# Performance work log

Measured on AMD Instinct MI355X. Metric: run time of the kernel, lower is better.

## Reference

```python
import jax, jax.numpy as jnp
import numpy as np

# Paired binary-tree layout over 20 inputs: widths 20->10->5->3->2->1.
# Odd trailing element is carried through unchanged. Node counts per layer
# sum to 19 nodes per tree; 19 trees total.
LAYER_WIDTHS = [20, 10, 5, 3, 2]  # widths at the input of each pairing layer
NODE_COUNTS = [10, 5, 2, 1, 1]    # pairs formed at each layer (sum = 19)
EPS = 1e-6


def setup_inputs() -> dict:
    key = jax.random.key(0)
    k1, k2, k3, k4 = jax.random.split(key, 4)
    B = 1_000_000
    p1 = jax.random.randint(k1, (B,), 0, 10)
    p2 = jax.random.randint(k2, (B,), 0, 10)
    c20 = jax.random.uniform(k3, (B, 20), dtype=jnp.float32)  # fuzzy truth values in [0,1]
    # raw andness params: one per node (19) per tree (19)
    w_raw = jax.random.normal(k4, (19, 19), dtype=jnp.float32)
    return {"p1": p1, "p2": p2, "c20": c20, "w_raw": w_raw}


def _multi_tree_forward(c20, w_raw):
    B = c20.shape[0]
    T = 19  # number of trees
    # andness in (0,1): convex mix between AND (min) and OR (max)
    w = jax.nn.sigmoid(w_raw)  # [T, 19]
    # all 19 trees see the same 20D input -> vectorize trees as a dim
    x = jnp.broadcast_to(c20[:, None, :], (B, T, 20))  # [B, T, 20]
    off = 0
    for width, n in zip(LAYER_WIDTHS, NODE_COUNTS):
        a = x[:, :, 0:2 * n:2]   # left children  [B, T, n]
        b = x[:, :, 1:2 * n:2]   # right children [B, T, n]
        wn = w[:, off:off + n][None, :, :]  # [1, T, n]
        y = wn * jnp.minimum(a, b) + (1.0 - wn) * jnp.maximum(a, b)
        if width % 2 == 1:  # carry the unpaired trailing element through
            y = jnp.concatenate([y, x[:, :, -1:]], axis=-1)
        x = y
        off += n
    out = x[:, :, 0]  # [B, 19] root of each tree
    return jnp.clip(out, EPS, 1.0 - EPS)


def reference(p1, p2, c20, w_raw):
    # p1/p2 are part of the original signature but unused by the forward math
    return _multi_tree_forward(c20, w_raw)
```

## Files before the change

### kernel.cpp

```cpp
#include <hip/hip_runtime.h>

#define EPS_F 1e-6f
#define BLK   256

typedef float v4f __attribute__((ext_vector_type(4)));

__global__ void sigmoid_w_kernel(const float* __restrict__ w_raw,
                                 float* __restrict__ w) {
    int i = threadIdx.x;
    if (i < 361) {
        w[i] = 1.0f / (1.0f + expf(-w_raw[i]));
    }
}

__device__ __forceinline__ float mixf(float a, float b, float wv) {
    float mn = fminf(a, b);
    float mx = fmaxf(a, b);
    return fmaf(wv, mn - mx, mx);
}

__device__ __forceinline__ float clampf(float r) {
    return __builtin_amdgcn_fmed3f(r, EPS_F, 1.0f - EPS_F);
}

__global__ __launch_bounds__(BLK, 4) void tree_forward_kernel(
    const float* __restrict__ c20,
    const float* __restrict__ w,
    float* __restrict__ out,
    int B)
{
    __shared__ float si[BLK * 20];
    __shared__ float so[BLK * 19];

    const int tid = threadIdx.x;
    const int S0  = blockIdx.x * BLK;

    {
        const v4f* g4 = reinterpret_cast<const v4f*>(c20) + (size_t)S0 * 5;
        v4f* s4 = reinterpret_cast<v4f*>(si);
        const int lim4  = B * 5;
        const int base4 = S0 * 5;
        #pragma unroll
        for (int j = 0; j < 5; ++j) {
            int idx = tid + j * BLK;
            v4f v;
            if (base4 + idx < lim4) {
                v = g4[idx];
            } else {
                v.x = 0.f; v.y = 0.f; v.z = 0.f; v.w = 0.f;
            }
            s4[idx] = v;
        }
    }
    __syncthreads();

    float mx[10], d[10];
    {
        const v4f* r4 = reinterpret_cast<const v4f*>(si + tid * 20);
        #pragma unroll
        for (int q = 0; q < 5; ++q) {
            v4f v = r4[q];
            {
                float mn = fminf(v.x, v.y);
                mx[2*q] = fmaxf(v.x, v.y);
                d[2*q]  = mn - mx[2*q];
            }
            {
                float mn = fminf(v.z, v.w);
                mx[2*q+1] = fmaxf(v.z, v.w);
                d[2*q+1]  = mn - mx[2*q+1];
            }
        }
    }

    float* __restrict__ o = &so[tid * 19];

    #pragma unroll
    for (int tp = 0; tp < 9; ++tp) {
        const int t0 = 2 * tp, t1 = 2 * tp + 1;
        const float* wr0 = w + t0 * 19;
        const float* wr1 = w + t1 * 19;

        float y0[10], y1[10];
        #pragma unroll
        for (int k = 0; k < 10; ++k) {
            y0[k] = fmaf(wr0[k], d[k], mx[k]);
            y1[k] = fmaf(wr1[k], d[k], mx[k]);
        }

        float z0[5], z1[5];
        #pragma unroll
        for (int k = 0; k < 5; ++k) {
            z0[k] = mixf(y0[2*k], y0[2*k+1], wr0[10 + k]);
            z1[k] = mixf(y1[2*k], y1[2*k+1], wr1[10 + k]);
        }

        float u00 = mixf(z0[0], z0[1], wr0[15]);
        float u01 = mixf(z0[2], z0[3], wr0[16]);
        float u10 = mixf(z1[0], z1[1], wr1[15]);
        float u11 = mixf(z1[2], z1[3], wr1[16]);

        float v0 = mixf(u00, u01, wr0[17]);
        float v1 = mixf(u10, u11, wr1[17]);

        float r0 = mixf(v0, z0[4], wr0[18]);
        float r1 = mixf(v1, z1[4], wr1[18]);

        o[t0] = clampf(r0);
        o[t1] = clampf(r1);
    }

    {
        const float* wr = w + 18 * 19;
        float y[10];
        #pragma unroll
        for (int k = 0; k < 10; ++k)
            y[k] = fmaf(wr[k], d[k], mx[k]);
        float z[5];
        #pragma unroll
        for (int k = 0; k < 5; ++k)
            z[k] = mixf(y[2*k], y[2*k+1], wr[10 + k]);
        float u0 = mixf(z[0], z[1], wr[15]);
        float u1 = mixf(z[2], z[3], wr[16]);
        float v0 = mixf(u0, u1, wr[17]);
        float r  = mixf(v0, z[4], wr[18]);
        o[18] = clampf(r);
    }

    __syncthreads();

    const int nDw    = B * 19;
    const int baseDw = S0 * 19;
    const v4f* ls = reinterpret_cast<const v4f*>(so);

    #pragma unroll
    for (int i = tid; i < (BLK * 19) / 4; i += BLK) {
        int g = baseDw + i * 4;
        if (g + 3 < nDw) {
            __builtin_nontemporal_store(ls[i], reinterpret_cast<v4f*>(out + g));
        } else if (g < nDw) {
            v4f v4 = ls[i];
            out[g] = v4.x;
            if (g + 1 < nDw) out[g + 1] = v4.y;
            if (g + 2 < nDw) out[g + 2] = v4.z;
        }
    }
}

extern "C" void kernel_launch(void* const* d_in, const int* in_sizes, int n_in,
                              void* d_out, int out_size, void* d_ws, size_t ws_size,
                              hipStream_t stream) {
    const float* c20   = (const float*)d_in[2];
    const float* w_raw = (const float*)d_in[3];
    float* out = (float*)d_out;
    float* w   = (float*)d_ws;

    int B = in_sizes[0];

    sigmoid_w_kernel<<<1, 384, 0, stream>>>(w_raw, w);

    int grid = (B + BLK - 1) / BLK;
    tree_forward_kernel<<<grid, BLK, 0, stream>>>(c20, w, out, B);
}
```

Measured before the change: 159.7 us.

## Load inputs directly per thread, process two samples per thread, wave-local output staging

Drops the shared-memory staging of the input rows. Each thread now loads its own 20-float rows straight from global memory with vector loads, and processes two samples (512 per block), with both rows' loads issued up front. Output is still staged in shared memory, but each wave copies out only its own 64 rows under wave barriers instead of a block-wide __syncthreads. The aim is to remove block syncs and an LDS round-trip and to raise memory-level parallelism. The cost is strided, uncoalesced 80-byte-per-thread global loads, more registers, and a reliance on the LDS write-then-read ordering holding within a wave.

```diff
diff --git a/kernel.cpp b/kernel.cpp
--- a/kernel.cpp
+++ b/kernel.cpp
@@ -2,6 +2,7 @@
 
 #define EPS_F 1e-6f
 #define BLK   256
+#define TPB   512
 
 typedef float v4f __attribute__((ext_vector_type(4)));
 
@@ -23,58 +24,26 @@
     return __builtin_amdgcn_fmed3f(r, EPS_F, 1.0f - EPS_F);
 }
 
-__global__ __launch_bounds__(BLK, 4) void tree_forward_kernel(
-    const float* __restrict__ c20,
-    const float* __restrict__ w,
-    float* __restrict__ out,
-    int B)
-{
-    __shared__ float si[BLK * 20];
-    __shared__ float so[BLK * 19];
-
-    const int tid = threadIdx.x;
-    const int S0  = blockIdx.x * BLK;
-
-    {
-        const v4f* g4 = reinterpret_cast<const v4f*>(c20) + (size_t)S0 * 5;
-        v4f* s4 = reinterpret_cast<v4f*>(si);
-        const int lim4  = B * 5;
-        const int base4 = S0 * 5;
-        #pragma unroll
-        for (int j = 0; j < 5; ++j) {
-            int idx = tid + j * BLK;
-            v4f v;
-            if (base4 + idx < lim4) {
-                v = g4[idx];
-            } else {
-                v.x = 0.f; v.y = 0.f; v.z = 0.f; v.w = 0.f;
-            }
-            s4[idx] = v;
+__device__ __forceinline__ void layer0(const v4f in[5], float d[10], float mx[10]) {
+    #pragma unroll
+    for (int q = 0; q < 5; ++q) {
+        v4f v = in[q];
+        {
+            float mn = fminf(v.x, v.y);
+            mx[2*q] = fmaxf(v.x, v.y);
+            d[2*q]  = mn - mx[2*q];
+        }
+        {
+            float mn = fminf(v.z, v.w);
+            mx[2*q+1] = fmaxf(v.z, v.w);
+            d[2*q+1]  = mn - mx[2*q+1];
         }
     }
-    __syncthreads();
+}
 
-    float mx[10], d[10];
-    {
-        const v4f* r4 = reinterpret_cast<const v4f*>(si + tid * 20);
-        #pragma unroll
-        for (int q = 0; q < 5; ++q) {
-            v4f v = r4[q];
-            {
-                float mn = fminf(v.x, v.y);
-                mx[2*q] = fmaxf(v.x, v.y);
-                d[2*q]  = mn - mx[2*q];
-            }
-            {
-                float mn = fminf(v.z, v.w);
-                mx[2*q+1] = fmaxf(v.z, v.w);
-                d[2*q+1]  = mn - mx[2*q+1];
-            }
-        }
-    }
-
-    float* __restrict__ o = &so[tid * 19];
-
+__device__ __forceinline__ void trees19(const float* __restrict__ w,
+                                        const float d[10], const float mx[10],
+                                        float* __restrict__ dst) {
     #pragma unroll
     for (int tp = 0; tp < 9; ++tp) {
         const int t0 = 2 * tp, t1 = 2 * tp + 1;
@@ -87,29 +56,23 @@
             y0[k] = fmaf(wr0[k], d[k], mx[k]);
             y1[k] = fmaf(wr1[k], d[k], mx[k]);
         }
-
         float z0[5], z1[5];
         #pragma unroll
         for (int k = 0; k < 5; ++k) {
             z0[k] = mixf(y0[2*k], y0[2*k+1], wr0[10 + k]);
             z1[k] = mixf(y1[2*k], y1[2*k+1], wr1[10 + k]);
         }
-
         float u00 = mixf(z0[0], z0[1], wr0[15]);
         float u01 = mixf(z0[2], z0[3], wr0[16]);
         float u10 = mixf(z1[0], z1[1], wr1[15]);
         float u11 = mixf(z1[2], z1[3], wr1[16]);
-
         float v0 = mixf(u00, u01, wr0[17]);
         float v1 = mixf(u10, u11, wr1[17]);
-
         float r0 = mixf(v0, z0[4], wr0[18]);
         float r1 = mixf(v1, z1[4], wr1[18]);
-
-        o[t0] = clampf(r0);
-        o[t1] = clampf(r1);
+        dst[t0] = clampf(r0);
+        dst[t1] = clampf(r1);
     }
-
     {
         const float* wr = w + 18 * 19;
         float y[10];
@@ -124,27 +87,82 @@
         float u1 = mixf(z[2], z[3], wr[16]);
         float v0 = mixf(u0, u1, wr[17]);
         float r  = mixf(v0, z[4], wr[18]);
-        o[18] = clampf(r);
+        dst[18] = clampf(r);
+    }
+}
+
+__device__ __forceinline__ void waveCopyOut(const float* __restrict__ soW,
+                                            float* __restrict__ out,
+                                            int baseDw, int nDw, int ln) {
+    const v4f* ls = reinterpret_cast<const v4f*>(soW);
+    #pragma unroll
+    for (int j = 0; j < 5; ++j) {
+        int idx = ln + j * 64;
+        if (idx < 304) {
+            int g = baseDw + idx * 4;
+            if (g + 3 < nDw) {
+                __builtin_nontemporal_store(ls[idx], reinterpret_cast<v4f*>(out + g));
+            } else if (g < nDw) {
+                v4f t = ls[idx];
+                out[g] = t.x;
+                if (g + 1 < nDw) out[g + 1] = t.y;
+                if (g + 2 < nDw) out[g + 2] = t.z;
+            }
+        }
+    }
+}
+
+__global__ __launch_bounds__(BLK, 4) void tree_forward_kernel(
+    const float* __restrict__ c20,
+    const float* __restrict__ w,
+    float* __restrict__ out,
+    int B)
+{
+    __shared__ float so[BLK * 19];
+
+    const int tid = threadIdx.x;
+    const int wv  = tid >> 6;
+    const int ln  = tid & 63;
+    const int S0  = blockIdx.x * TPB;
+    const int sA  = S0 + tid;
+    const int sB  = sA + BLK;
+
+    v4f ia[5], ib[5];
+    {
+        const v4f* pA = reinterpret_cast<const v4f*>(c20 + (size_t)sA * 20);
+        const v4f* pB = reinterpret_cast<const v4f*>(c20 + (size_t)sB * 20);
+        const bool vA = (sA < B), vB = (sB < B);
+        #pragma unroll
+        for (int q = 0; q < 5; ++q) {
+            v4f z; z.x = 0.f; z.y = 0.f; z.z = 0.f; z.w = 0.f;
+            ia[q] = vA ? pA[q] : z;
+        }
+        #pragma unroll
+        for (int q = 0; q < 5; ++q) {
+            v4f z; z.x = 0.f; z.y = 0.f; z.z = 0.f; z.w = 0.f;
+            ib[q] = vB ? pB[q] : z;
+        }
     }
 
-    __syncthreads();
+    float* __restrict__ o   = &so[tid * 19];
+    const float* __restrict__ soW = &so[(wv * 64) * 19];
+    const int nDw = B * 19;
 
-    const int nDw    = B * 19;
-    const int baseDw = S0 * 19;
-    const v4f* ls = reinterpret_cast<const v4f*>(so);
+    float d[10], mx[10];
 
-    #pragma unroll
-    for (int i = tid; i < (BLK * 19) / 4; i += BLK) {
-        int g = baseDw + i * 4;
-        if (g + 3 < nDw) {
-            __builtin_nontemporal_store(ls[i], reinterpret_cast<v4f*>(out + g));
-        } else if (g < nDw) {
-            v4f v4 = ls[i];
-            out[g] = v4.x;
-            if (g + 1 < nDw) out[g + 1] = v4.y;
-            if (g + 2 < nDw) out[g + 2] = v4.z;
-        }
-    }
+    layer0(ia, d, mx);
+    trees19(w, d, mx, o);
+    __builtin_amdgcn_wave_barrier();
+    asm volatile("s_waitcnt lgkmcnt(0)" ::: "memory");
+    __builtin_amdgcn_wave_barrier();
+    waveCopyOut(soW, out, (S0 + wv * 64) * 19, nDw, ln);
+
+    layer0(ib, d, mx);
+    trees19(w, d, mx, o);
+    __builtin_amdgcn_wave_barrier();
+    asm volatile("s_waitcnt lgkmcnt(0)" ::: "memory");
+    __builtin_amdgcn_wave_barrier();
+    waveCopyOut(soW, out, (S0 + BLK + wv * 64) * 19, nDw, ln);
 }
 
 extern "C" void kernel_launch(void* const* d_in, const int* in_sizes, int n_in,
@@ -159,6 +177,6 @@
 
     sigmoid_w_kernel<<<1, 384, 0, stream>>>(w_raw, w);
 
-    int grid = (B + BLK - 1) / BLK;
+    int grid = (B + TPB - 1) / TPB;
     tree_forward_kernel<<<grid, BLK, 0, stream>>>(c20, w, out, B);
 }
```

Result: no change. 160.2 us (+0.3%).
